# Kernel tuning notes

Measured on AMD Instinct MI355X. Metric: run time of the kernel, lower is better.

## Reference

```python
import jax, jax.numpy as jnp
import numpy as np

S, N, F = 32, 512, 256        # systems, atoms per system, feature/charge channels
R_EXCL = 5.0                  # neighbor_list_options.cutoff -> exclusion_radius
BOX = 30.0                    # box edge for random positions (Angstrom-scale)


def setup_inputs() -> dict:
    key = jax.random.key(0)
    k1, k2, k3, k4 = jax.random.split(key, 4)
    positions = jax.random.uniform(k1, (S, N, 3), dtype=jnp.float32) * BOX
    features = jax.random.normal(k2, (S * N, F), dtype=jnp.float32)
    W = jax.random.normal(k3, (F, F), dtype=jnp.float32) / jnp.sqrt(F)
    b = jax.random.normal(k4, (F,), dtype=jnp.float32) * 0.01
    return {"positions": positions, "features": features, "W": W, "b": b}


def _pair_potential(d):
    # CoulombPotential(smearing=None, exclusion_radius=R_EXCL).from_dist:
    # v(r) = (1/r) * (1 - f_cut(r)),  f_cut = 0.5*(1 + cos(pi*r/R_EXCL)) for r < R_EXCL
    fcut = jnp.where(d < R_EXCL, 0.5 * (1.0 + jnp.cos(jnp.pi * d / R_EXCL)), 0.0)
    return (1.0 / d) * (1.0 - fcut)


def reference(positions, features, W, b):
    # charges_map: Linear(F, F)
    charges = features @ W.T + b                      # [S*N, F]
    q = charges.reshape(S, N, F)                      # per-system charges

    # all-pairs distances per system (torch.combinations path, both directions
    # accumulated by the half-neighbor-list Calculator)
    diff = positions[:, :, None, :] - positions[:, None, :, :]   # [S,N,N,3]
    d = jnp.sqrt(jnp.sum(diff * diff, axis=-1))                  # [S,N,N]
    eye = jnp.eye(N, dtype=bool)
    d_safe = jnp.where(eye, 1.0, d)
    v = jnp.where(eye, 0.0, _pair_potential(d_safe))             # [S,N,N]

    # V_i = 0.5 * sum_j v(r_ij) q_j  (torchpme energy convention E = sum_i q_i V_i)
    V = 0.5 * jnp.einsum('sij,sjf->sif', v, q)                   # [S,N,F]

    # module returns potential * charges, concatenated over systems
    return (V * q).reshape(S * N, F)
```

## Files before the change

kernel.cpp:

```cpp
#include <hip/hip_runtime.h>
#include <hip/hip_cooperative_groups.h>

#define SY 32
#define NA 512
#define FD 256

typedef __attribute__((ext_vector_type(8))) short bf16x8;
typedef __attribute__((ext_vector_type(4))) short bf16x4;
typedef __attribute__((ext_vector_type(4))) float f32x4;

static __device__ __forceinline__ short f2bf(float x) {
    union { float f; unsigned u; } v; v.f = x;
    unsigned r = v.u + 0x7fffu + ((v.u >> 16) & 1u);
    return (short)(r >> 16);
}
static __device__ __forceinline__ float bf2f(short x) {
    union { float f; unsigned u; } v;
    v.u = ((unsigned)(unsigned short)x) << 16;
    return v.f;
}

__global__ __launch_bounds__(256) void prep_w(
    const float* __restrict__ W, short* __restrict__ Wb)
{
    int idx = (blockIdx.x * 256 + threadIdx.x) * 4;
    float4 v = *(const float4*)&W[idx];
    bf16x4 p; p[0] = f2bf(v.x); p[1] = f2bf(v.y);
              p[2] = f2bf(v.z); p[3] = f2bf(v.w);
    *(bf16x4*)&Wb[idx] = p;
}

__global__ __launch_bounds__(512) void charges_v25(
    const float* __restrict__ feat, const float* __restrict__ Wfp,
    const short* __restrict__ Wb, const float* __restrict__ b,
    float* __restrict__ qfp, short* __restrict__ qT)
{
    __shared__ __attribute__((aligned(16))) short sA[64 * 72];
    __shared__ __attribute__((aligned(16))) short sB[256 * 72];
    const int t    = threadIdx.x;
    const int i0   = blockIdx.x * 64;
    const int w    = t >> 6;
    const int lane = t & 63;
    const int n16  = lane & 15;
    const int quad = lane >> 4;

    f32x4 acc[4][2];
    #pragma unroll
    for (int a = 0; a < 4; ++a)
        #pragma unroll
        for (int c = 0; c < 2; ++c) acc[a][c] = (f32x4)0.0f;

    for (int k0 = 0; k0 < FD; k0 += 64) {
        #pragma unroll
        for (int m = 0; m < 2; ++m) {
            int lin = t + 512 * m;
            int row = lin >> 4, kq = lin & 15;
            float4 v = *(const float4*)&feat[(size_t)(i0 + row) * FD + k0 + 4 * kq];
            bf16x4 p; p[0] = f2bf(v.x); p[1] = f2bf(v.y);
                      p[2] = f2bf(v.z); p[3] = f2bf(v.w);
            *(bf16x4*)&sA[row * 72 + 4 * kq] = p;
        }
        if (Wb) {
            #pragma unroll
            for (int n = 0; n < 4; ++n) {
                int S = t + 512 * n;
                int f = S >> 3, c = S & 7;
                uint4 v = *(const uint4*)&Wb[(size_t)f * FD + k0 + c * 8];
                *(uint4*)&sB[f * 72 + c * 8] = v;
            }
        } else {
            #pragma unroll
            for (int m = 0; m < 8; ++m) {
                int lin = t + 512 * m;
                int f = lin >> 4, kq = lin & 15;
                float4 v = *(const float4*)&Wfp[(size_t)f * FD + k0 + 4 * kq];
                bf16x4 p; p[0] = f2bf(v.x); p[1] = f2bf(v.y);
                          p[2] = f2bf(v.z); p[3] = f2bf(v.w);
                *(bf16x4*)&sB[f * 72 + 4 * kq] = p;
            }
        }
        __syncthreads();

        #pragma unroll
        for (int ks = 0; ks < 64; ks += 32) {
            bf16x8 af[4], bfr[2];
            #pragma unroll
            for (int it = 0; it < 4; ++it)
                af[it] = *(const bf16x8*)&sA[(16 * it + n16) * 72 + ks + quad * 8];
            #pragma unroll
            for (int fb = 0; fb < 2; ++fb)
                bfr[fb] = *(const bf16x8*)&sB[(32 * w + 16 * fb + n16) * 72 + ks + quad * 8];
            #pragma unroll
            for (int it = 0; it < 4; ++it)
                #pragma unroll
                for (int fb = 0; fb < 2; ++fb)
                    acc[it][fb] = __builtin_amdgcn_mfma_f32_16x16x32_bf16(
                        af[it], bfr[fb], acc[it][fb], 0, 0, 0);
        }
        __syncthreads();
    }

    float bias[2];
    #pragma unroll
    for (int fb = 0; fb < 2; ++fb) bias[fb] = b[32 * w + 16 * fb + n16];

    if (qfp) {
        #pragma unroll
        for (int it = 0; it < 4; ++it)
            #pragma unroll
            for (int fb = 0; fb < 2; ++fb)
                #pragma unroll
                for (int r = 0; r < 4; ++r) {
                    int i = i0 + 16 * it + 4 * quad + r;
                    int f = 32 * w + 16 * fb + n16;
                    qfp[(size_t)i * FD + f] = acc[it][fb][r] + bias[fb];
                }
    }

    if (qT) {
        short* tr = sB;
        #pragma unroll
        for (int it = 0; it < 4; ++it)
            #pragma unroll
            for (int fb = 0; fb < 2; ++fb) {
                bf16x4 p;
                #pragma unroll
                for (int r = 0; r < 4; ++r) p[r] = f2bf(acc[it][fb][r] + bias[fb]);
                int f = 32 * w + 16 * fb + n16;
                *(bf16x4*)&tr[f * 72 + 16 * it + 4 * quad] = p;
            }
        __syncthreads();
        short* qTs = qT + ((size_t)(i0 >> 9)) * FD * NA;
        const int ilb = i0 & 511;
        #pragma unroll
        for (int n = 0; n < 4; ++n) {
            int S = t + 512 * n;
            int f = S >> 3;
            int c = S & 7;
            uint4 v = *(const uint4*)&tr[f * 72 + c * 8];
            *(uint4*)&qTs[(size_t)f * NA + ilb + c * 8] = v;
        }
    }
}

__global__ __launch_bounds__(256) void lr_fast(
    const float* __restrict__ pos, float* __restrict__ out,
    const short* __restrict__ qT)
{
    __shared__ float px[NA], py[NA], pz[NA];
    __shared__ __attribute__((aligned(16))) short sqb[FD * 64];
    __shared__ __attribute__((aligned(16))) short svb[32 * 64];

    const int blk = blockIdx.x;
    const int s   = blk & 31;
    const int i0  = (blk >> 5) * 32;
    const int t   = threadIdx.x;
    const int w    = t >> 6;
    const int lane = t & 63;
    const int n16  = lane & 15;
    const int quad = lane >> 4;

    for (int m = t; m < NA; m += 256) {
        const float* p = &pos[((size_t)s * NA + m) * 3];
        px[m] = p[0]; py[m] = p[1]; pz[m] = p[2];
    }

    f32x4 acc[2][4];
    #pragma unroll
    for (int a = 0; a < 2; ++a)
        #pragma unroll
        for (int c = 0; c < 4; ++c) acc[a][c] = (f32x4)0.0f;
    float qreg[2][4][4];

    const short* qTs = qT + (size_t)s * FD * NA;
    const int pi = t & 31;
    const int pc = t >> 5;
    const int gi = i0 + pi;

    __syncthreads();
    const float xi = px[gi], yi = py[gi], zi = pz[gi];

    for (int j0 = 0; j0 < NA; j0 += 64) {
        #pragma unroll
        for (int n = 0; n < 8; ++n) {
            int S  = n * 256 + t;
            int f  = S >> 3;
            int cs = S & 7;
            int c  = (cs - f) & 7;
            uint4 v = *(const uint4*)&qTs[(size_t)f * NA + j0 + c * 8];
            *(uint4*)&sqb[f * 64 + cs * 8] = v;
        }
        bf16x8 vrow;
        #pragma unroll
        for (int jj = 0; jj < 8; ++jj) {
            int gj = j0 + pc * 8 + jj;
            float dx = xi - px[gj];
            float dy = yi - py[gj];
            float dz = zi - pz[gj];
            float r2 = dx * dx + dy * dy + dz * dz;
            float inv = __builtin_amdgcn_rsqf(r2);
            float dd  = r2 * inv;
            float sn = __sinf(dd * 0.31415926535f);
            float om = (dd < 5.0f) ? sn * sn : 1.0f;
            float vv = (gi != gj) ? 0.5f * om * inv : 0.0f;
            vrow[jj] = f2bf(vv);
        }
        *(bf16x8*)&svb[pi * 64 + (((pc + pi) & 7) * 8)] = vrow;
        __syncthreads();

        if (j0 == (i0 & ~63)) {
            const int jb0 = i0 & 63;
            #pragma unroll
            for (int it = 0; it < 2; ++it)
                #pragma unroll
                for (int fb = 0; fb < 4; ++fb) {
                    int f = 64 * w + 16 * fb + n16;
                    #pragma unroll
                    for (int r = 0; r < 4; ++r) {
                        int jl = jb0 + 16 * it + 4 * quad + r;
                        int c  = jl >> 3, o = jl & 7;
                        qreg[it][fb][r] =
                            bf2f(sqb[f * 64 + (((c + f) & 7) * 8) + o]);
                    }
                }
        }

        bf16x8 af[2][2], bfr[2][4];
        #pragma unroll
        for (int it = 0; it < 2; ++it)
            #pragma unroll
            for (int kh = 0; kh < 2; ++kh) {
                int i = 16 * it + n16;
                int c = kh * 4 + quad;
                af[it][kh] = *(const bf16x8*)&svb[i * 64 + (((c + i) & 7) * 8)];
            }
        #pragma unroll
        for (int fb = 0; fb < 4; ++fb)
            #pragma unroll
            for (int kh = 0; kh < 2; ++kh) {
                int f = 64 * w + 16 * fb + n16;
                int c = kh * 4 + quad;
                bfr[kh][fb] = *(const bf16x8*)&sqb[f * 64 + (((c + f) & 7) * 8)];
            }
        #pragma unroll
        for (int kh = 0; kh < 2; ++kh)
            #pragma unroll
            for (int it = 0; it < 2; ++it)
                #pragma unroll
                for (int fb = 0; fb < 4; ++fb)
                    acc[it][fb] = __builtin_amdgcn_mfma_f32_16x16x32_bf16(
                        af[it][kh], bfr[kh][fb], acc[it][fb], 0, 0, 0);
        __syncthreads();
    }

    #pragma unroll
    for (int it = 0; it < 2; ++it)
        #pragma unroll
        for (int fb = 0; fb < 4; ++fb)
            #pragma unroll
            for (int r = 0; r < 4; ++r) {
                int i = i0 + 16 * it + 4 * quad + r;
                int f = 64 * w + 16 * fb + n16;
                size_t a = ((size_t)s * NA + i) * FD + f;
                out[a] = acc[it][fb][r] * qreg[it][fb][r];
            }
}

__global__ __launch_bounds__(256) void lr_coop(
    const float* __restrict__ pos, float* __restrict__ gbuf)
{
    __shared__ float px[NA], py[NA], pz[NA];
    __shared__ __attribute__((aligned(16))) short svb[64 * 40];
    __shared__ __attribute__((aligned(16))) short sqb[FD * 40];

    const int blk = blockIdx.x;
    const int s   = blk & 31;
    const int i0  = (blk >> 5) * 64;
    const int t   = threadIdx.x;
    const int w    = t >> 6;
    const int lane = t & 63;
    const int n16  = lane & 15;
    const int quad = lane >> 4;

    for (int m = t; m < NA; m += 256) {
        const float* p = &pos[((size_t)s * NA + m) * 3];
        px[m] = p[0]; py[m] = p[1]; pz[m] = p[2];
    }

    f32x4 acc[4][4];
    #pragma unroll
    for (int a = 0; a < 4; ++a)
        #pragma unroll
        for (int c = 0; c < 4; ++c) acc[a][c] = (f32x4)0.0f;

    __syncthreads();

    const int fq  = t >> 2;
    const int jb  = t & 3;
    const int iv  = t & 63;
    const int jbv = t >> 6;
    const int gi  = i0 + iv;

    float4 rq[8];
    #pragma unroll
    for (int m = 0; m < 8; ++m)
        rq[m] = *(const float4*)&gbuf[((size_t)s * NA + 8 * jb + m) * FD + 4 * fq];

    for (int j0 = 0; j0 < NA; j0 += 32) {
        bf16x8 vrow;
        #pragma unroll
        for (int jj = 0; jj < 8; ++jj) {
            int gj = j0 + 8 * jbv + jj;
            float dx = px[gi] - px[gj];
            float dy = py[gi] - py[gj];
            float dz = pz[gi] - pz[gj];
            float dd = sqrtf(dx * dx + dy * dy + dz * dz);
            float om = (dd < 5.0f) ? 0.5f * (1.0f - __cosf(dd * 0.62831853071795f))
                                   : 1.0f;
            float vv = (gi != gj) ? (0.5f * om * __builtin_amdgcn_rcpf(dd)) : 0.0f;
            vrow[jj] = f2bf(vv);
        }
        bf16x8 rows[4];
        #pragma unroll
        for (int m = 0; m < 8; ++m) {
            rows[0][m] = f2bf(rq[m].x);
            rows[1][m] = f2bf(rq[m].y);
            rows[2][m] = f2bf(rq[m].z);
            rows[3][m] = f2bf(rq[m].w);
        }
        #pragma unroll
        for (int d = 0; d < 4; ++d) {
            int f = 4 * fq + d;
            int phys = (jb + (f >> 3)) & 3;
            *(bf16x8*)&sqb[f * 40 + phys * 8] = rows[d];
        }
        {
            int phys = (jbv + (iv >> 3)) & 3;
            *(bf16x8*)&svb[iv * 40 + phys * 8] = vrow;
        }
        {
            int jn = (j0 + 32) & (NA - 1);
            #pragma unroll
            for (int m = 0; m < 8; ++m)
                rq[m] = *(const float4*)&gbuf[((size_t)s * NA + jn + 8 * jb + m) * FD + 4 * fq];
        }
        __syncthreads();

        bf16x8 af[4], bfr[4];
        #pragma unroll
        for (int it = 0; it < 4; ++it) {
            int i = 16 * it + n16;
            int phys = (quad + (i >> 3)) & 3;
            af[it] = *(const bf16x8*)&svb[i * 40 + phys * 8];
        }
        #pragma unroll
        for (int fb = 0; fb < 4; ++fb) {
            int f = 16 * (4 * w + fb) + n16;
            int phys = (quad + (f >> 3)) & 3;
            bfr[fb] = *(const bf16x8*)&sqb[f * 40 + phys * 8];
        }
        #pragma unroll
        for (int it = 0; it < 4; ++it)
            #pragma unroll
            for (int fb = 0; fb < 4; ++fb)
                acc[it][fb] = __builtin_amdgcn_mfma_f32_16x16x32_bf16(
                    af[it], bfr[fb], acc[it][fb], 0, 0, 0);
        __syncthreads();
    }

    cooperative_groups::this_grid().sync();

    #pragma unroll
    for (int it = 0; it < 4; ++it)
        #pragma unroll
        for (int fb = 0; fb < 4; ++fb)
            #pragma unroll
            for (int r = 0; r < 4; ++r) {
                int i = i0 + 16 * it + 4 * quad + r;
                int f = 16 * (4 * w + fb) + n16;
                size_t a = ((size_t)s * NA + i) * FD + f;
                gbuf[a] = acc[it][fb][r] * gbuf[a];
            }
}

extern "C" void kernel_launch(void* const* d_in, const int* in_sizes, int n_in,
                              void* d_out, int out_size, void* d_ws, size_t ws_size,
                              hipStream_t stream) {
    const float* positions = (const float*)d_in[0];
    const float* features  = (const float*)d_in[1];
    const float* W         = (const float*)d_in[2];
    const float* b         = (const float*)d_in[3];
    float* gbuf = (float*)d_out;

    const size_t qT_elems = (size_t)SY * NA * FD;
    const size_t need = (qT_elems + FD * FD) * sizeof(short);
    const bool fast = (ws_size >= need);

    if (fast) {
        short* qT = (short*)d_ws;
        short* Wb = (short*)d_ws + qT_elems;
        prep_w<<<dim3(64), 256, 0, stream>>>(W, Wb);
        charges_v25<<<dim3(256), 512, 0, stream>>>(features, W, Wb, b, nullptr, qT);
        lr_fast<<<dim3(512), 256, 0, stream>>>(positions, gbuf, qT);
    } else {
        charges_v25<<<dim3(256), 512, 0, stream>>>(features, W, nullptr, b, gbuf, nullptr);
        void* args[] = {(void*)&positions, (void*)&gbuf};
        hipLaunchCooperativeKernel((void*)lr_coop, dim3(256), dim3(256),
                                   args, 0, stream);
    }
}
```

Baseline: 112.8 us.

## Retile lr_fast to 64-row by 128-feature blocks with the whole q slice preloaded in LDS

Each block of lr_fast now covers 64 atoms by 128 feature channels instead of 32 atoms by all 256 channels. It preloads that block's entire 128x512 bf16 charge slice into shared memory once, with a rotated layout, rather than streaming q tiles on every j step. The final q multiplier is read straight from global memory at the end. This halves how often q is re-read across blocks, but each pair potential is now computed twice (once per feature half). Shared memory grows to about 142 KB per block, which limits occupancy to one block per CU, and the up-front load is not overlapped with compute.

```diff
diff --git a/kernel.cpp b/kernel.cpp
--- a/kernel.cpp
+++ b/kernel.cpp
@@ -148,12 +148,14 @@
     const short* __restrict__ qT)
 {
     __shared__ float px[NA], py[NA], pz[NA];
-    __shared__ __attribute__((aligned(16))) short sqb[FD * 64];
-    __shared__ __attribute__((aligned(16))) short svb[32 * 64];
+    __shared__ __attribute__((aligned(16))) short sqb[128 * NA];
+    __shared__ __attribute__((aligned(16))) short svb[64 * 64];
 
     const int blk = blockIdx.x;
     const int s   = blk & 31;
-    const int i0  = (blk >> 5) * 32;
+    const int rr  = blk >> 5;
+    const int f0  = (rr & 1) * 128;
+    const int i0  = (rr >> 1) * 64;
     const int t   = threadIdx.x;
     const int w    = t >> 6;
     const int lane = t & 63;
@@ -165,105 +167,106 @@
         px[m] = p[0]; py[m] = p[1]; pz[m] = p[2];
     }
 
-    f32x4 acc[2][4];
-    #pragma unroll
-    for (int a = 0; a < 2; ++a)
-        #pragma unroll
-        for (int c = 0; c < 4; ++c) acc[a][c] = (f32x4)0.0f;
-    float qreg[2][4][4];
-
-    const short* qTs = qT + (size_t)s * FD * NA;
-    const int pi = t & 31;
-    const int pc = t >> 5;
-    const int gi = i0 + pi;
+    f32x4 acc[4][2];
+    #pragma unroll
+    for (int a = 0; a < 4; ++a)
+        #pragma unroll
+        for (int c = 0; c < 2; ++c) acc[a][c] = (f32x4)0.0f;
+
+    const short* qTs = qT + (size_t)s * FD * NA + (size_t)f0 * NA;
+
+    #pragma unroll
+    for (int g = 0; g < 4; ++g) {
+        uint4 v[8];
+        #pragma unroll
+        for (int n = 0; n < 8; ++n) {
+            int S  = t + 256 * (8 * g + n);
+            int fl = S >> 6;
+            int cs = S & 63;
+            int c  = (cs - fl) & 63;
+            v[n] = *(const uint4*)&qTs[(size_t)fl * NA + c * 8];
+        }
+        #pragma unroll
+        for (int n = 0; n < 8; ++n) {
+            int S  = t + 256 * (8 * g + n);
+            int fl = S >> 6;
+            int cs = S & 63;
+            *(uint4*)&sqb[fl * NA + cs * 8] = v[n];
+        }
+    }
+
+    const int pi  = t & 63;
+    const int pjc = t >> 6;
+    const int gi  = i0 + pi;
 
     __syncthreads();
     const float xi = px[gi], yi = py[gi], zi = pz[gi];
 
     for (int j0 = 0; j0 < NA; j0 += 64) {
         #pragma unroll
-        for (int n = 0; n < 8; ++n) {
-            int S  = n * 256 + t;
-            int f  = S >> 3;
-            int cs = S & 7;
-            int c  = (cs - f) & 7;
-            uint4 v = *(const uint4*)&qTs[(size_t)f * NA + j0 + c * 8];
-            *(uint4*)&sqb[f * 64 + cs * 8] = v;
-        }
-        bf16x8 vrow;
-        #pragma unroll
-        for (int jj = 0; jj < 8; ++jj) {
-            int gj = j0 + pc * 8 + jj;
-            float dx = xi - px[gj];
-            float dy = yi - py[gj];
-            float dz = zi - pz[gj];
-            float r2 = dx * dx + dy * dy + dz * dz;
-            float inv = __builtin_amdgcn_rsqf(r2);
-            float dd  = r2 * inv;
-            float sn = __sinf(dd * 0.31415926535f);
-            float om = (dd < 5.0f) ? sn * sn : 1.0f;
-            float vv = (gi != gj) ? 0.5f * om * inv : 0.0f;
-            vrow[jj] = f2bf(vv);
-        }
-        *(bf16x8*)&svb[pi * 64 + (((pc + pi) & 7) * 8)] = vrow;
-        __syncthreads();
-
-        if (j0 == (i0 & ~63)) {
-            const int jb0 = i0 & 63;
-            #pragma unroll
-            for (int it = 0; it < 2; ++it)
-                #pragma unroll
-                for (int fb = 0; fb < 4; ++fb) {
-                    int f = 64 * w + 16 * fb + n16;
-                    #pragma unroll
-                    for (int r = 0; r < 4; ++r) {
-                        int jl = jb0 + 16 * it + 4 * quad + r;
-                        int c  = jl >> 3, o = jl & 7;
-                        qreg[it][fb][r] =
-                            bf2f(sqb[f * 64 + (((c + f) & 7) * 8) + o]);
-                    }
-                }
-        }
-
-        bf16x8 af[2][2], bfr[2][4];
-        #pragma unroll
-        for (int it = 0; it < 2; ++it)
+        for (int h = 0; h < 2; ++h) {
+            bf16x8 vr;
+            #pragma unroll
+            for (int jj = 0; jj < 8; ++jj) {
+                int gj = j0 + pjc * 16 + h * 8 + jj;
+                float dx = xi - px[gj];
+                float dy = yi - py[gj];
+                float dz = zi - pz[gj];
+                float r2 = dx * dx + dy * dy + dz * dz;
+                float inv = __builtin_amdgcn_rsqf(r2);
+                float dd  = r2 * inv;
+                float sn = __sinf(dd * 0.31415926535f);
+                float om = (dd < 5.0f) ? sn * sn : 1.0f;
+                float vv = (gi != gj) ? 0.5f * om * inv : 0.0f;
+                vr[jj] = f2bf(vv);
+            }
+            int c = pjc * 2 + h;
+            *(bf16x8*)&svb[pi * 64 + (((c + pi) & 7) * 8)] = vr;
+        }
+        __syncthreads();
+
+        bf16x8 af[4][2], bfr[2][2];
+        #pragma unroll
+        for (int it = 0; it < 4; ++it)
             #pragma unroll
             for (int kh = 0; kh < 2; ++kh) {
                 int i = 16 * it + n16;
                 int c = kh * 4 + quad;
                 af[it][kh] = *(const bf16x8*)&svb[i * 64 + (((c + i) & 7) * 8)];
             }
-        #pragma unroll
-        for (int fb = 0; fb < 4; ++fb)
+        const int jc0 = j0 >> 3;
+        #pragma unroll
+        for (int fb = 0; fb < 2; ++fb)
             #pragma unroll
             for (int kh = 0; kh < 2; ++kh) {
-                int f = 64 * w + 16 * fb + n16;
-                int c = kh * 4 + quad;
-                bfr[kh][fb] = *(const bf16x8*)&sqb[f * 64 + (((c + f) & 7) * 8)];
+                int fl = 32 * w + 16 * fb + n16;
+                int cg = jc0 + kh * 4 + quad;
+                bfr[kh][fb] = *(const bf16x8*)&sqb[fl * NA + (((cg + fl) & 63) * 8)];
             }
         #pragma unroll
         for (int kh = 0; kh < 2; ++kh)
             #pragma unroll
-            for (int it = 0; it < 2; ++it)
+            for (int it = 0; it < 4; ++it)
                 #pragma unroll
-                for (int fb = 0; fb < 4; ++fb)
+                for (int fb = 0; fb < 2; ++fb)
                     acc[it][fb] = __builtin_amdgcn_mfma_f32_16x16x32_bf16(
                         af[it][kh], bfr[kh][fb], acc[it][fb], 0, 0, 0);
         __syncthreads();
     }
 
     #pragma unroll
-    for (int it = 0; it < 2; ++it)
-        #pragma unroll
-        for (int fb = 0; fb < 4; ++fb)
+    for (int it = 0; it < 4; ++it)
+        #pragma unroll
+        for (int fb = 0; fb < 2; ++fb) {
+            int fl = 32 * w + 16 * fb + n16;
+            bf16x4 p = *(const bf16x4*)&qTs[(size_t)fl * NA + i0 + 16 * it + 4 * quad];
             #pragma unroll
             for (int r = 0; r < 4; ++r) {
                 int i = i0 + 16 * it + 4 * quad + r;
-                int f = 64 * w + 16 * fb + n16;
-                size_t a = ((size_t)s * NA + i) * FD + f;
-                out[a] = acc[it][fb][r] * qreg[it][fb][r];
-            }
+                size_t a = ((size_t)s * NA + i) * FD + f0 + fl;
+                out[a] = acc[it][fb][r] * bf2f(p[r]);
+            }
+        }
 }
 
 __global__ __launch_bounds__(256) void lr_coop(
```

Result: no change. 111.0 us (-1.6%).
